# Performance work log

Measured on AMD Instinct MI355X. Metric: run time of the kernel, lower is better.

The kernel has to match this reference:

```python
import jax, jax.numpy as jnp
import numpy as np

FP8_MAX = 448.0


def setup_inputs() -> dict:
    key = jax.random.key(0)
    kx, kw = jax.random.split(key)
    in_features, out_features = 1024, 1024
    x = jax.random.normal(kx, (32768, in_features), dtype=jnp.float32)
    # kaiming_uniform_ with a=sqrt(5): bound = sqrt(6/((1+a^2)*fan_in)) = sqrt(1/fan_in)
    bound = 1.0 / np.sqrt(in_features)
    weight = jax.random.uniform(kw, (out_features, in_features), dtype=jnp.float32,
                                minval=-bound, maxval=bound)
    bias = jnp.zeros((out_features,), dtype=jnp.float32)
    return {"x": x, "weight": weight, "bias": bias}


def reference(x, weight, bias):
    # per-tensor input quant
    input_scale = jnp.maximum(jnp.max(jnp.abs(x)) / FP8_MAX, 1e-12)
    x_q = jnp.round(jnp.clip(x / input_scale, -FP8_MAX, FP8_MAX))
    # per-output-channel weight quant
    weight_amax = jnp.max(jnp.abs(weight), axis=1)            # [out]
    weight_scale = jnp.maximum(weight_amax / FP8_MAX, 1e-12)  # [out]
    weight_q = jnp.round(jnp.clip(weight / weight_scale[:, None], -FP8_MAX, FP8_MAX))
    # integer-valued GEMM in fp32, then dequant + bias
    output_q = jnp.einsum('ti,oi->to', x_q, weight_q)          # [T, out]
    output = output_q * (input_scale * weight_scale)[None, :]
    return output + bias
```

## Files before the change

kernel.cpp:

```cpp
#include <hip/hip_runtime.h>
#include <hip/hip_fp16.h>

#define FP8_MAX 448.0f
#define M_ 32768
#define N_ 1024
#define K_ 1024
#define BM 128
#define BN 128
#define BK 64

typedef _Float16 f16x8 __attribute__((ext_vector_type(8)));
typedef _Float16 f16x4 __attribute__((ext_vector_type(4)));
typedef __fp16  h16x2 __attribute__((ext_vector_type(2)));
typedef float f32x16 __attribute__((ext_vector_type(16)));

__device__ inline void gload_lds16(const void* g, void* l) {
    __builtin_amdgcn_global_load_lds(
        (const __attribute__((address_space(1))) void*)g,
        (__attribute__((address_space(3))) void*)l,
        16, 0, 0);
}

__device__ inline f16x8 quant8(float4 v0, float4 v1, float inv) {
    h16x2 t0 = __builtin_amdgcn_cvt_pkrtz(rintf(v0.x * inv), rintf(v0.y * inv));
    h16x2 t1 = __builtin_amdgcn_cvt_pkrtz(rintf(v0.z * inv), rintf(v0.w * inv));
    h16x2 t2 = __builtin_amdgcn_cvt_pkrtz(rintf(v1.x * inv), rintf(v1.y * inv));
    h16x2 t3 = __builtin_amdgcn_cvt_pkrtz(rintf(v1.z * inv), rintf(v1.w * inv));
    f16x8 q;
    q[0] = (_Float16)t0[0]; q[1] = (_Float16)t0[1];
    q[2] = (_Float16)t1[0]; q[3] = (_Float16)t1[1];
    q[4] = (_Float16)t2[0]; q[5] = (_Float16)t2[1];
    q[6] = (_Float16)t3[0]; q[7] = (_Float16)t3[1];
    return q;
}

__global__ __launch_bounds__(256) void prep_kernel(const float* __restrict__ x,
                                                   const float* __restrict__ w,
                                                   float* __restrict__ xamax_part,
                                                   float* __restrict__ wscale,
                                                   _Float16* __restrict__ wq,
                                                   int n) {
    __shared__ float sm[4];
    if (blockIdx.x < 1024) {
        int row = blockIdx.x;
        const float4* wr4 = (const float4*)(w + (size_t)row * K_);
        float4 v = wr4[threadIdx.x];
        float m = fmaxf(fmaxf(fabsf(v.x), fabsf(v.y)), fmaxf(fabsf(v.z), fabsf(v.w)));
        #pragma unroll
        for (int off = 32; off > 0; off >>= 1)
            m = fmaxf(m, __shfl_down(m, off, 64));
        if ((threadIdx.x & 63) == 0) sm[threadIdx.x >> 6] = m;
        __syncthreads();
        m = fmaxf(fmaxf(sm[0], sm[1]), fmaxf(sm[2], sm[3]));
        float scale = fmaxf(m / FP8_MAX, 1e-12f);
        if (threadIdx.x == 0) wscale[row] = scale;
        float inv = 1.0f / scale;
        f16x4 o;
        o[0] = (_Float16)rintf(fminf(fmaxf(v.x * inv, -FP8_MAX), FP8_MAX));
        o[1] = (_Float16)rintf(fminf(fmaxf(v.y * inv, -FP8_MAX), FP8_MAX));
        o[2] = (_Float16)rintf(fminf(fmaxf(v.z * inv, -FP8_MAX), FP8_MAX));
        o[3] = (_Float16)rintf(fminf(fmaxf(v.w * inv, -FP8_MAX), FP8_MAX));
        ((f16x4*)(wq + (size_t)row * K_))[threadIdx.x] = o;
    } else {
        float m = 0.0f;
        const float4* x4 = (const float4*)x;
        int n4 = n >> 2;
        int stride = 2048 * 256;
        for (int i = (blockIdx.x - 1024) * 256 + threadIdx.x; i < n4; i += stride) {
            float4 v = x4[i];
            m = fmaxf(m, fmaxf(fmaxf(fabsf(v.x), fabsf(v.y)),
                               fmaxf(fabsf(v.z), fabsf(v.w))));
        }
        #pragma unroll
        for (int off = 32; off > 0; off >>= 1)
            m = fmaxf(m, __shfl_down(m, off, 64));
        if ((threadIdx.x & 63) == 0) sm[threadIdx.x >> 6] = m;
        __syncthreads();
        if (threadIdx.x == 0) {
            xamax_part[blockIdx.x - 1024] =
                fmaxf(fmaxf(sm[0], sm[1]), fmaxf(sm[2], sm[3]));
        }
    }
}

__global__ __launch_bounds__(256) void gemm_kernel(const float* __restrict__ x,
                                                   const _Float16* __restrict__ wq,
                                                   const float* __restrict__ xamax_part,
                                                   const float* __restrict__ wscale,
                                                   const float* __restrict__ bias,
                                                   float* __restrict__ out) {
    __shared__ __align__(16) _Float16 sA[2][BM * BK];
    __shared__ __align__(16) _Float16 sB[BN * BK];

    const int tid = threadIdx.x;

    const float4* p4 = (const float4*)xamax_part;
    float4 pa = p4[tid];
    float4 pb = p4[tid + 256];
    float m = fmaxf(fmaxf(fmaxf(pa.x, pa.y), fmaxf(pa.z, pa.w)),
                    fmaxf(fmaxf(pb.x, pb.y), fmaxf(pb.z, pb.w)));
    #pragma unroll
    for (int off = 32; off > 0; off >>= 1)
        m = fmaxf(m, __shfl_down(m, off, 64));
    float* red = (float*)sA;
    if ((tid & 63) == 0) red[tid >> 6] = m;
    __syncthreads();
    const float amax = fmaxf(fmaxf(red[0], red[1]), fmaxf(red[2], red[3]));
    __syncthreads();
    const float iscale = fmaxf(amax / FP8_MAX, 1e-12f);
    const float inv = 1.0f / iscale;

    const int wave = tid >> 6;
    const int lane = tid & 63;
    const int h   = lane >> 5;
    const int m32 = lane & 31;
    const int m7  = m32 & 7;
    const int wm = (wave >> 1) * 64;
    const int wn = (wave & 1) * 64;

    const int bb = (int)blockIdx.x;
    const int n0 = (((bb >> 3) & 7)) * BN;
    const int m0 = (((bb >> 6) << 3) + (bb & 7)) * BM;

    const int trow = tid >> 3;
    const int tcol = (((tid & 7) ^ (trow & 7)) * 8);
    const _Float16* Bg = wq + ((size_t)(n0 + trow)) * K_ + tcol;
    char* lB = (char*)sB + wave * 1024;

    const int arow = tid >> 3;
    const int ach  = tid & 7;
    const float* Ag = x + (size_t)(m0 + arow) * K_ + ach * 8;
    _Float16* Aw0 = (_Float16*)sA + (size_t)arow * BK + ((ach ^ (arow & 7)) * 8);

    f32x16 acc[2][2] = {};
    float4 pv[4][2];

    #pragma unroll
    for (int rr = 0; rr < 4; ++rr) {
        const float* src = Ag + (size_t)(rr * 32) * K_;
        pv[rr][0] = *(const float4*)src;
        pv[rr][1] = *(const float4*)(src + 4);
    }
    #pragma unroll
    for (int rr = 0; rr < 4; ++rr)
        *(f16x8*)(Aw0 + (size_t)(rr * 32) * BK) = quant8(pv[rr][0], pv[rr][1], inv);

    int buf = 0;
    for (int kt = 0; kt < K_; kt += BK) {
        #pragma unroll
        for (int rr = 0; rr < 4; ++rr)
            gload_lds16(Bg + kt + (size_t)(rr * 32) * K_, lB + rr * 4096);
        const int kn = (kt + BK) & (K_ - 1);
        #pragma unroll
        for (int rr = 0; rr < 4; ++rr) {
            const float* src = Ag + kn + (size_t)(rr * 32) * K_;
            pv[rr][0] = *(const float4*)src;
            pv[rr][1] = *(const float4*)(src + 4);
        }
        __syncthreads();

        const _Float16* sAb = (const _Float16*)sA + (size_t)buf * (BM * BK);
        #pragma unroll
        for (int ks = 0; ks < 4; ++ks) {
            f16x8 a[2], b[2];
            const int chunk = ks * 2 + h;
            const int pos = (chunk ^ m7) * 8;
            #pragma unroll
            for (int i = 0; i < 2; ++i)
                a[i] = *(const f16x8*)&sAb[(wm + i * 32 + m32) * BK + pos];
            #pragma unroll
            for (int j = 0; j < 2; ++j)
                b[j] = *(const f16x8*)&sB[(wn + j * 32 + m32) * BK + pos];
            #pragma unroll
            for (int i = 0; i < 2; ++i)
                #pragma unroll
                for (int j = 0; j < 2; ++j)
                    acc[i][j] = __builtin_amdgcn_mfma_f32_32x32x16_f16(a[i], b[j], acc[i][j], 0, 0, 0);
        }
        __syncthreads();

        if (kt + BK < K_) {
            _Float16* Awn = Aw0 + (size_t)(buf ^ 1) * (BM * BK);
            #pragma unroll
            for (int rr = 0; rr < 4; ++rr)
                *(f16x8*)(Awn + (size_t)(rr * 32) * BK) = quant8(pv[rr][0], pv[rr][1], inv);
            buf ^= 1;
        }
    }

    #pragma unroll
    for (int j = 0; j < 2; ++j) {
        int col = n0 + wn + j * 32 + m32;
        float sc = iscale * wscale[col];
        float bs = bias[col];
        #pragma unroll
        for (int i = 0; i < 2; ++i) {
            int rb = m0 + wm + i * 32 + 4 * h;
            #pragma unroll
            for (int reg = 0; reg < 16; ++reg) {
                int row = rb + (reg & 3) + 8 * (reg >> 2);
                out[(size_t)row * N_ + col] = acc[i][j][reg] * sc + bs;
            }
        }
    }
}

extern "C" void kernel_launch(void* const* d_in, const int* in_sizes, int n_in,
                              void* d_out, int out_size, void* d_ws, size_t ws_size,
                              hipStream_t stream) {
    const float* x    = (const float*)d_in[0];
    const float* w    = (const float*)d_in[1];
    const float* bias = (const float*)d_in[2];
    float* out = (float*)d_out;

    char* ws = (char*)d_ws;
    float* xamax_part  = (float*)(ws + 1024);
    float* wscale      = (float*)(ws + 16384);
    _Float16* wq       = (_Float16*)(ws + 32768);

    prep_kernel<<<3072, 256, 0, stream>>>(x, w, xamax_part, wscale, wq, M_ * K_);
    gemm_kernel<<<2048, 256, 0, stream>>>(x, wq, xamax_part, wscale, bias, out);
}
```

Before: 316.9 us.

## Double-buffer weight tiles and unroll GEMM K-loop by two with ping-pong register sets

Weight tiles get a second LDS buffer, and the K loop is unrolled by two with separate register sets for the prefetched activation rows. The next tile's direct-to-LDS weight load can then be issued before the current tile's MFMAs, and each half-step needs one barrier instead of two. The first tile loads are also issued before the global amax reduction so their latency overlaps it. The cost is more LDS per block and more registers held for prefetch, which could lower occupancy. The loop also issues wrap-around loads on the last iteration that are never used.

```diff
diff --git a/kernel.cpp b/kernel.cpp
--- a/kernel.cpp
+++ b/kernel.cpp
@@ -32,6 +32,28 @@
     q[4] = (_Float16)t2[0]; q[5] = (_Float16)t2[1];
     q[6] = (_Float16)t3[0]; q[7] = (_Float16)t3[1];
     return q;
+}
+
+__device__ inline void mfma_tile(const _Float16* sAb, const _Float16* sBb,
+                                 f32x16 acc[2][2],
+                                 int wm, int wn, int m32, int m7, int h) {
+    #pragma unroll
+    for (int ks = 0; ks < 4; ++ks) {
+        f16x8 a[2], b[2];
+        const int chunk = ks * 2 + h;
+        const int pos = (chunk ^ m7) * 8;
+        #pragma unroll
+        for (int i = 0; i < 2; ++i)
+            a[i] = *(const f16x8*)&sAb[(wm + i * 32 + m32) * BK + pos];
+        #pragma unroll
+        for (int j = 0; j < 2; ++j)
+            b[j] = *(const f16x8*)&sBb[(wn + j * 32 + m32) * BK + pos];
+        #pragma unroll
+        for (int i = 0; i < 2; ++i)
+            #pragma unroll
+            for (int j = 0; j < 2; ++j)
+                acc[i][j] = __builtin_amdgcn_mfma_f32_32x32x16_f16(a[i], b[j], acc[i][j], 0, 0, 0);
+    }
 }
 
 __global__ __launch_bounds__(256) void prep_kernel(const float* __restrict__ x,
@@ -90,26 +112,9 @@
                                                    const float* __restrict__ bias,
                                                    float* __restrict__ out) {
     __shared__ __align__(16) _Float16 sA[2][BM * BK];
-    __shared__ __align__(16) _Float16 sB[BN * BK];
+    __shared__ __align__(16) _Float16 sB[2][BN * BK];
 
     const int tid = threadIdx.x;
-
-    const float4* p4 = (const float4*)xamax_part;
-    float4 pa = p4[tid];
-    float4 pb = p4[tid + 256];
-    float m = fmaxf(fmaxf(fmaxf(pa.x, pa.y), fmaxf(pa.z, pa.w)),
-                    fmaxf(fmaxf(pb.x, pb.y), fmaxf(pb.z, pb.w)));
-    #pragma unroll
-    for (int off = 32; off > 0; off >>= 1)
-        m = fmaxf(m, __shfl_down(m, off, 64));
-    float* red = (float*)sA;
-    if ((tid & 63) == 0) red[tid >> 6] = m;
-    __syncthreads();
-    const float amax = fmaxf(fmaxf(red[0], red[1]), fmaxf(red[2], red[3]));
-    __syncthreads();
-    const float iscale = fmaxf(amax / FP8_MAX, 1e-12f);
-    const float inv = 1.0f / iscale;
-
     const int wave = tid >> 6;
     const int lane = tid & 63;
     const int h   = lane >> 5;
@@ -119,73 +124,100 @@
     const int wn = (wave & 1) * 64;
 
     const int bb = (int)blockIdx.x;
-    const int n0 = (((bb >> 3) & 7)) * BN;
+    const int n0 = ((bb >> 3) & 7) * BN;
     const int m0 = (((bb >> 6) << 3) + (bb & 7)) * BM;
 
     const int trow = tid >> 3;
     const int tcol = (((tid & 7) ^ (trow & 7)) * 8);
     const _Float16* Bg = wq + ((size_t)(n0 + trow)) * K_ + tcol;
-    char* lB = (char*)sB + wave * 1024;
+    char* lB0 = (char*)&sB[0][0] + wave * 1024;
+    char* lB1 = (char*)&sB[1][0] + wave * 1024;
 
     const int arow = tid >> 3;
     const int ach  = tid & 7;
     const float* Ag = x + (size_t)(m0 + arow) * K_ + ach * 8;
-    _Float16* Aw0 = (_Float16*)sA + (size_t)arow * BK + ((ach ^ (arow & 7)) * 8);
-
-    f32x16 acc[2][2] = {};
-    float4 pv[4][2];
-
+    _Float16* Aw0 = &sA[0][0] + (size_t)arow * BK + ((ach ^ (arow & 7)) * 8);
+    _Float16* Aw1 = Aw0 + BM * BK;
+
+    float4 pvA[4][2], pvB[4][2];
+
+    #pragma unroll
+    for (int rr = 0; rr < 4; ++rr)
+        gload_lds16(Bg + (size_t)(rr * 32) * K_, lB0 + rr * 4096);
     #pragma unroll
     for (int rr = 0; rr < 4; ++rr) {
         const float* src = Ag + (size_t)(rr * 32) * K_;
-        pv[rr][0] = *(const float4*)src;
-        pv[rr][1] = *(const float4*)(src + 4);
-    }
+        pvA[rr][0] = *(const float4*)src;
+        pvA[rr][1] = *(const float4*)(src + 4);
+    }
+
+    const float4* p4 = (const float4*)xamax_part;
+    float4 pa = p4[tid];
+    float4 pb = p4[tid + 256];
+    float m = fmaxf(fmaxf(fmaxf(pa.x, pa.y), fmaxf(pa.z, pa.w)),
+                    fmaxf(fmaxf(pb.x, pb.y), fmaxf(pb.z, pb.w)));
+    #pragma unroll
+    for (int off = 32; off > 0; off >>= 1)
+        m = fmaxf(m, __shfl_down(m, off, 64));
+    float* red = (float*)&sA[0][0];
+    if ((tid & 63) == 0) red[tid >> 6] = m;
+    __syncthreads();
+    const float amax = fmaxf(fmaxf(red[0], red[1]), fmaxf(red[2], red[3]));
+    __syncthreads();
+    const float iscale = fmaxf(amax / FP8_MAX, 1e-12f);
+    const float inv = 1.0f / iscale;
+
     #pragma unroll
     for (int rr = 0; rr < 4; ++rr)
-        *(f16x8*)(Aw0 + (size_t)(rr * 32) * BK) = quant8(pv[rr][0], pv[rr][1], inv);
-
-    int buf = 0;
-    for (int kt = 0; kt < K_; kt += BK) {
+        *(f16x8*)(Aw0 + (size_t)(rr * 32) * BK) = quant8(pvA[rr][0], pvA[rr][1], inv);
+    #pragma unroll
+    for (int rr = 0; rr < 4; ++rr) {
+        const float* src = Ag + BK + (size_t)(rr * 32) * K_;
+        pvB[rr][0] = *(const float4*)src;
+        pvB[rr][1] = *(const float4*)(src + 4);
+    }
+
+    f32x16 acc[2][2] = {};
+
+    for (int kt = 0; kt < K_; kt += 2 * BK) {
+        __syncthreads();
         #pragma unroll
         for (int rr = 0; rr < 4; ++rr)
-            gload_lds16(Bg + kt + (size_t)(rr * 32) * K_, lB + rr * 4096);
-        const int kn = (kt + BK) & (K_ - 1);
-        #pragma unroll
-        for (int rr = 0; rr < 4; ++rr) {
-            const float* src = Ag + kn + (size_t)(rr * 32) * K_;
-            pv[rr][0] = *(const float4*)src;
-            pv[rr][1] = *(const float4*)(src + 4);
-        }
-        __syncthreads();
-
-        const _Float16* sAb = (const _Float16*)sA + (size_t)buf * (BM * BK);
-        #pragma unroll
-        for (int ks = 0; ks < 4; ++ks) {
-            f16x8 a[2], b[2];
-            const int chunk = ks * 2 + h;
-            const int pos = (chunk ^ m7) * 8;
-            #pragma unroll
-            for (int i = 0; i < 2; ++i)
-                a[i] = *(const f16x8*)&sAb[(wm + i * 32 + m32) * BK + pos];
-            #pragma unroll
-            for (int j = 0; j < 2; ++j)
-                b[j] = *(const f16x8*)&sB[(wn + j * 32 + m32) * BK + pos];
-            #pragma unroll
-            for (int i = 0; i < 2; ++i)
-                #pragma unroll
-                for (int j = 0; j < 2; ++j)
-                    acc[i][j] = __builtin_amdgcn_mfma_f32_32x32x16_f16(a[i], b[j], acc[i][j], 0, 0, 0);
-        }
-        __syncthreads();
-
-        if (kt + BK < K_) {
-            _Float16* Awn = Aw0 + (size_t)(buf ^ 1) * (BM * BK);
+            gload_lds16(Bg + (kt + BK) + (size_t)(rr * 32) * K_, lB1 + rr * 4096);
+        {
+            const int kA = (kt + 2 * BK) & (K_ - 1);
+            #pragma unroll
+            for (int rr = 0; rr < 4; ++rr) {
+                const float* src = Ag + kA + (size_t)(rr * 32) * K_;
+                pvA[rr][0] = *(const float4*)src;
+                pvA[rr][1] = *(const float4*)(src + 4);
+            }
+        }
+        asm volatile("" ::: "memory");
+        mfma_tile(&sA[0][0], &sB[0][0], acc, wm, wn, m32, m7, h);
+        #pragma unroll
+        for (int rr = 0; rr < 4; ++rr)
+            *(f16x8*)(Aw1 + (size_t)(rr * 32) * BK) = quant8(pvB[rr][0], pvB[rr][1], inv);
+
+        __syncthreads();
+        {
+            const int kB = (kt + 2 * BK) & (K_ - 1);
             #pragma unroll
             for (int rr = 0; rr < 4; ++rr)
-                *(f16x8*)(Awn + (size_t)(rr * 32) * BK) = quant8(pv[rr][0], pv[rr][1], inv);
-            buf ^= 1;
-        }
+                gload_lds16(Bg + kB + (size_t)(rr * 32) * K_, lB0 + rr * 4096);
+            const int kA = (kt + 3 * BK) & (K_ - 1);
+            #pragma unroll
+            for (int rr = 0; rr < 4; ++rr) {
+                const float* src = Ag + kA + (size_t)(rr * 32) * K_;
+                pvB[rr][0] = *(const float4*)src;
+                pvB[rr][1] = *(const float4*)(src + 4);
+            }
+        }
+        asm volatile("" ::: "memory");
+        mfma_tile(&sA[1][0], &sB[1][0], acc, wm, wn, m32, m7, h);
+        #pragma unroll
+        for (int rr = 0; rr < 4; ++rr)
+            *(f16x8*)(Aw0 + (size_t)(rr * 32) * BK) = quant8(pvA[rr][0], pvA[rr][1], inv);
     }
 
     #pragma unroll
```

Result: no change. 319.9 us (+0.9%).
